# Optimization experiments

Measured on AMD Instinct MI355X. Metric: run time of the kernel, lower is better.

The kernel has to match this reference:

```python
import jax, jax.numpy as jnp
import numpy as np

N_NODES = 50000
N_EDGES = 800000
IN_DIM = 89
HID = 128


def gcn_conv(x, src, dst, deg_inv_sqrt, W, b):
    # PyG GCNConv: x' = D^{-1/2} (A + I) D^{-1/2} (x W) + b
    h = x @ W  # [N, F_out]
    norm = deg_inv_sqrt[src] * deg_inv_sqrt[dst]  # per-edge norm [E]
    msgs = h[src] * norm[:, None]  # gather + scale [E, F_out]
    agg = jax.ops.segment_sum(msgs, dst, num_segments=x.shape[0])
    # self-loop contribution: norm = deg_inv_sqrt[i]^2
    agg = agg + h * (deg_inv_sqrt * deg_inv_sqrt)[:, None]
    return agg + b


def setup_inputs() -> dict:
    key = jax.random.key(0)
    k1, k2, k3, k4, k5, k6 = jax.random.split(key, 6)
    x = jax.random.normal(k1, (N_NODES, IN_DIM), dtype=jnp.float32)
    edge_index = jax.random.randint(k2, (2, N_EDGES), 0, N_NODES, dtype=jnp.int64)
    # Glorot-style init for GCN weights
    W1 = jax.random.normal(k3, (IN_DIM, HID), dtype=jnp.float32) * (1.0 / np.sqrt(IN_DIM))
    b1 = jnp.zeros((HID,), dtype=jnp.float32)
    W2 = jax.random.normal(k4, (HID, HID), dtype=jnp.float32) * (1.0 / np.sqrt(HID))
    b2 = jnp.zeros((HID,), dtype=jnp.float32)
    return {"x": x, "edge_index": edge_index, "W1": W1, "b1": b1, "W2": W2, "b2": b2}


def reference(x, edge_index, W1, b1, W2, b2):
    src = edge_index[0]
    dst = edge_index[1]
    n = x.shape[0]
    # degree of A + I: 1 (self loop) + in-degree
    deg = 1.0 + jax.ops.segment_sum(jnp.ones((src.shape[0],), x.dtype), dst, num_segments=n)
    deg_inv_sqrt = jax.lax.rsqrt(deg)
    h = jax.nn.relu(gcn_conv(x, src, dst, deg_inv_sqrt, W1, b1))
    h = jax.nn.relu(gcn_conv(h, src, dst, deg_inv_sqrt, W2, b2))
    return (h, edge_index)
```

## Files before the change

### kernel.cpp

```cpp
#include <hip/hip_runtime.h>
#include <hip/hip_bf16.h>


#define HID 128
#define KIN 89
#define KP1 96
#define KP2 128
#define BSH 7
#define BNODES 128
#define MAXBUCK 512
#define NPB 128
#define P4CAP 3072

typedef __attribute__((ext_vector_type(8))) short bf16x8;
typedef __attribute__((ext_vector_type(4))) float f32x4;

static __device__ inline float2 unpack_bf16(unsigned v) {
    union { unsigned u; float f; } lo, hi;
    lo.u = v << 16;
    hi.u = v & 0xFFFF0000u;
    return make_float2(lo.f, hi.f);
}

static __device__ inline unsigned pack_bf16(float a, float b) {
    __hip_bfloat162 h = __float22bfloat162_rn(make_float2(a, b));
    return *reinterpret_cast<unsigned*>(&h);
}

static __device__ inline unsigned short f2bf(float v) {
    __hip_bfloat16 h = __float2bfloat16(v);
    return *reinterpret_cast<unsigned short*>(&h);
}

__global__ __launch_bounds__(256) void p1_kernel(
    const int* __restrict__ ei,
    int* __restrict__ histG,
    const float* __restrict__ W1, unsigned short* __restrict__ W1t,
    const float* __restrict__ W2, unsigned short* __restrict__ W2t,
    int E, int nbuck)
{
    __shared__ int h[MAXBUCK];
    const int tid = threadIdx.x, blk = blockIdx.x;
    const int* dst = ei + E;
    for (int b = tid; b < nbuck; b += 256) h[b] = 0;

    int tg = blk * 256 + tid;
    if (tg < HID * KP1) {
        int n = tg / KP1, k = tg % KP1;
        W1t[tg] = f2bf(k < KIN ? W1[(size_t)k * HID + n] : 0.0f);
    } else {
        int t2 = tg - HID * KP1;
        if (t2 < HID * HID) {
            int n = t2 / HID, k = t2 % HID;
            W2t[t2] = f2bf(W2[(size_t)k * HID + n]);
        }
    }
    __syncthreads();

    const int chunk = (E + NPB - 1) / NPB;
    const int beg = blk * chunk, end = min(beg + chunk, E);
    for (int i = beg + tid; i < end; i += 256)
        atomicAdd(&h[dst[i] >> BSH], 1);
    __syncthreads();
    for (int b = tid; b < nbuck; b += 256) histG[b * NPB + blk] = h[b];
}

__global__ __launch_bounds__(NPB) void p2a_kernel(
    int* __restrict__ histG, int* __restrict__ totals)
{
    __shared__ int wsum[NPB / 64];
    const int b = blockIdx.x, tid = threadIdx.x, lane = tid & 63, wid = tid >> 6;
    int c = histG[b * NPB + tid];
    int s = c;
#pragma unroll
    for (int off = 1; off < 64; off <<= 1) {
        int t = __shfl_up(s, off, 64);
        if (lane >= off) s += t;
    }
    if (lane == 63) wsum[wid] = s;
    __syncthreads();
    if (tid == 0) {
        int a = 0;
#pragma unroll
        for (int w = 0; w < NPB / 64; ++w) { int t = wsum[w]; wsum[w] = a; a += t; }
    }
    __syncthreads();
    int excl = wsum[wid] + s - c;
    histG[b * NPB + tid] = excl;
    if (tid == NPB - 1) totals[b] = excl + c;
}

static __device__ inline void scan_totals2(const int* __restrict__ totals,
                                           int* __restrict__ sexcl,
                                           int* __restrict__ wsum,
                                           int nbuck, int tid)
{
    const int lane = tid & 63, wid = tid >> 6;
    const int i0 = 2 * tid, i1 = 2 * tid + 1;
    int t0 = (i0 < nbuck) ? totals[i0] : 0;
    int t1 = (i1 < nbuck) ? totals[i1] : 0;
    int p = t0 + t1;
    int s = p;
#pragma unroll
    for (int off = 1; off < 64; off <<= 1) {
        int t = __shfl_up(s, off, 64);
        if (lane >= off) s += t;
    }
    if (lane == 63) wsum[wid] = s;
    __syncthreads();
    if (tid == 0) {
        int a = 0;
#pragma unroll
        for (int w = 0; w < 4; ++w) { int t = wsum[w]; wsum[w] = a; a += t; }
    }
    __syncthreads();
    int excl = wsum[wid] + s - p;
    sexcl[i0] = excl;
    sexcl[i1] = excl + t0;
}

__global__ __launch_bounds__(256) void p3_part_kernel(
    const int* __restrict__ ei, const int* __restrict__ histG,
    const int* __restrict__ totals, unsigned* __restrict__ ebuf,
    float* __restrict__ outE,
    int E, int nbuck)
{
    __shared__ int cur[MAXBUCK];
    __shared__ int wsum[4];
    const int tid = threadIdx.x, blk = blockIdx.x;
    const int* src = ei;
    const int* dst = ei + E;
    scan_totals2(totals, cur, wsum, nbuck, tid);
    __syncthreads();
    for (int b = tid; b < nbuck; b += 256) cur[b] += histG[b * NPB + blk];
    const int chunk = (E + NPB - 1) / NPB;
    const int beg = blk * chunk, end = min(beg + chunk, E);
    __syncthreads();
    for (int i = beg + tid; i < end; i += 256) {
        int sxi = src[i];
        int d = dst[i];
        int b = d >> BSH;
        int pos = atomicAdd(&cur[b], 1);
        ebuf[pos] = ((unsigned)(d & (BNODES - 1)) << 16) | (unsigned)sxi;
        outE[i] = (float)sxi;
        outE[E + i] = (float)d;
    }
}

__global__ __launch_bounds__(256) void p4_sort_kernel(
    const unsigned* __restrict__ ebuf, const int* __restrict__ totals,
    unsigned short* __restrict__ csr, int* __restrict__ rowptr,
    float* __restrict__ dis,
    const float* __restrict__ X, unsigned* __restrict__ Xhs,
    int N, int E, int nbuck)
{
    __shared__ int counts[BNODES];
    __shared__ int cursor[BNODES];
    __shared__ int sbase[MAXBUCK];
    __shared__ int wsum[4];
    __shared__ int w2[2];
    __shared__ unsigned short staging[P4CAP];
    const int b = blockIdx.x, tid = threadIdx.x, lane = tid & 63, wid = tid >> 6;

    scan_totals2(totals, sbase, wsum, nbuck, tid);
    __syncthreads();
    const int gbase = sbase[b];
    const int cnt = totals[b];

    if (tid < BNODES) counts[tid] = 0;
    __syncthreads();
    for (int i = tid; i < cnt; i += 256)
        atomicAdd(&counts[ebuf[gbase + i] >> 16], 1);
    __syncthreads();

    int c = 0, s = 0;
    if (tid < BNODES) {
        c = counts[tid];
        s = c;
#pragma unroll
        for (int off = 1; off < 64; off <<= 1) {
            int t = __shfl_up(s, off, 64);
            if (lane >= off) s += t;
        }
        if (lane == 63) w2[wid] = s;
    }
    __syncthreads();
    if (tid == 0) { int t = w2[0]; w2[0] = 0; w2[1] = t; }
    __syncthreads();
    if (tid < BNODES) {
        int excl = w2[wid] + s - c;
        cursor[tid] = excl;
        int node = b * BNODES + tid;
        if (node < N) {
            rowptr[node] = gbase + excl;
            dis[node] = rsqrtf(1.0f + (float)c);
        }
    }
    if (b == 0 && tid == 0) rowptr[N] = E;
    __syncthreads();

    if (cnt <= P4CAP) {
        for (int i = tid; i < cnt; i += 256) {
            unsigned v = ebuf[gbase + i];
            int pos = atomicAdd(&cursor[v >> 16], 1);
            staging[pos] = (unsigned short)(v & 0xFFFFu);
        }
        __syncthreads();
        for (int i = tid; i < cnt; i += 256)
            csr[gbase + i] = staging[i];
    } else {
        for (int i = tid; i < cnt; i += 256) {
            unsigned v = ebuf[gbase + i];
            int pos = atomicAdd(&cursor[v >> 16], 1);
            csr[gbase + pos] = (unsigned short)(v & 0xFFFFu);
        }
    }

    const int nloc = min(BNODES, N - b * BNODES);
    if (nloc > 0) {
        const int tot = nloc * (KP1 / 2);
        for (int i = tid; i < tot; i += 256) {
            int nl = i / (KP1 / 2), cc = i % (KP1 / 2);
            int node = b * BNODES + nl;
            float d = rsqrtf(1.0f + (float)counts[nl]);
            const float* xr = X + (size_t)node * KIN;
            float a = (2 * cc     < KIN) ? d * xr[2 * cc]     : 0.0f;
            float bb = (2 * cc + 1 < KIN) ? d * xr[2 * cc + 1] : 0.0f;
            Xhs[(size_t)node * (KP1 / 2) + cc] = pack_bf16(a, bb);
        }
    }
}

template<int KPA, bool LAYER1>
__global__ __launch_bounds__(256) void fused_kernel(
    const uint4* __restrict__ rows, const int* __restrict__ rowptr,
    const unsigned short* __restrict__ csr,
    const unsigned short* __restrict__ Wt, const float* __restrict__ bias,
    const float* __restrict__ dis, void* __restrict__ outp, int N)
{
    constexpr int ROWU4 = KPA / 8;
    constexpr int LDSP  = (KPA == 96) ? 104 : 136;
    __shared__ unsigned short lds_a[16][LDSP];
    const int tid  = threadIdx.x;
    const int wave = tid >> 6;
    const int lane = tid & 63;
    const int sub  = (lane >> 4) & 3;
    const int sl   = lane & 15;
    const int slc  = (ROWU4 == 16) ? sl : min(sl, ROWU4 - 1);
    const bool act = (ROWU4 == 16) || (sl < ROWU4);
    const int blk0 = blockIdx.x * 16;

    {
        const int lrow = wave * 4 + sub;
        const int node = blk0 + lrow;
        const bool valid = node < N;
        const int cn = valid ? node : N - 1;

        uint4 sv = rows[(size_t)cn * ROWU4 + slc];
        float a0, a1, a2, a3, a4, a5, a6, a7;
        {
            float2 q;
            q = unpack_bf16(sv.x); a0 = q.x; a1 = q.y;
            q = unpack_bf16(sv.y); a2 = q.x; a3 = q.y;
            q = unpack_bf16(sv.z); a4 = q.x; a5 = q.y;
            q = unpack_bf16(sv.w); a6 = q.x; a7 = q.y;
        }

        int beg = rowptr[cn];
        int end = valid ? rowptr[cn + 1] : beg;
        int j = beg;
        for (; j + 4 <= end; j += 4) {
            int r0 = csr[j], r1 = csr[j + 1], r2 = csr[j + 2], r3 = csr[j + 3];
            uint4 v0 = rows[(size_t)r0 * ROWU4 + slc];
            uint4 v1 = rows[(size_t)r1 * ROWU4 + slc];
            uint4 v2 = rows[(size_t)r2 * ROWU4 + slc];
            uint4 v3 = rows[(size_t)r3 * ROWU4 + slc];
            float2 q;
            q = unpack_bf16(v0.x); a0 += q.x; a1 += q.y;
            q = unpack_bf16(v0.y); a2 += q.x; a3 += q.y;
            q = unpack_bf16(v0.z); a4 += q.x; a5 += q.y;
            q = unpack_bf16(v0.w); a6 += q.x; a7 += q.y;
            q = unpack_bf16(v1.x); a0 += q.x; a1 += q.y;
            q = unpack_bf16(v1.y); a2 += q.x; a3 += q.y;
            q = unpack_bf16(v1.z); a4 += q.x; a5 += q.y;
            q = unpack_bf16(v1.w); a6 += q.x; a7 += q.y;
            q = unpack_bf16(v2.x); a0 += q.x; a1 += q.y;
            q = unpack_bf16(v2.y); a2 += q.x; a3 += q.y;
            q = unpack_bf16(v2.z); a4 += q.x; a5 += q.y;
            q = unpack_bf16(v2.w); a6 += q.x; a7 += q.y;
            q = unpack_bf16(v3.x); a0 += q.x; a1 += q.y;
            q = unpack_bf16(v3.y); a2 += q.x; a3 += q.y;
            q = unpack_bf16(v3.z); a4 += q.x; a5 += q.y;
            q = unpack_bf16(v3.w); a6 += q.x; a7 += q.y;
        }
        for (; j < end; ++j) {
            int r = csr[j];
            uint4 v = rows[(size_t)r * ROWU4 + slc];
            float2 q;
            q = unpack_bf16(v.x); a0 += q.x; a1 += q.y;
            q = unpack_bf16(v.y); a2 += q.x; a3 += q.y;
            q = unpack_bf16(v.z); a4 += q.x; a5 += q.y;
            q = unpack_bf16(v.w); a6 += q.x; a7 += q.y;
        }

        if (act) {
            uint4 pk = make_uint4(pack_bf16(a0, a1), pack_bf16(a2, a3),
                                  pack_bf16(a4, a5), pack_bf16(a6, a7));
            *(uint4*)&lds_a[lrow][sl * 8] = pk;
        }
    }
    __syncthreads();

    const int m    = lane & 15;
    const int quad = lane >> 4;
    const int node = blk0 + m;

    f32x4 acc[2];
    acc[0] = (f32x4){0.0f, 0.0f, 0.0f, 0.0f};
    acc[1] = (f32x4){0.0f, 0.0f, 0.0f, 0.0f};

    const unsigned short* arp = &lds_a[m][0];

#pragma unroll
    for (int c = 0; c < KPA / 32; ++c) {
        const int k0 = c * 32 + quad * 8;
        bf16x8 nv = *(const bf16x8*)(arp + k0);
#pragma unroll
        for (int t2 = 0; t2 < 2; ++t2) {
            const int t = wave * 2 + t2;
            bf16x8 wv = *(const bf16x8*)(Wt + (size_t)(t * 16 + m) * KPA + k0);
            acc[t2] = __builtin_amdgcn_mfma_f32_16x16x32_bf16(wv, nv, acc[t2], 0, 0, 0);
        }
    }

    if (node < N) {
        const float dv = dis[node];
#pragma unroll
        for (int t2 = 0; t2 < 2; ++t2) {
            const int col0 = (wave * 2 + t2) * 16 + quad * 4;
            float4 bb = *(const float4*)&bias[col0];
            float r0 = fmaxf(fmaf(dv, acc[t2][0], bb.x), 0.0f);
            float r1 = fmaxf(fmaf(dv, acc[t2][1], bb.y), 0.0f);
            float r2 = fmaxf(fmaf(dv, acc[t2][2], bb.z), 0.0f);
            float r3 = fmaxf(fmaf(dv, acc[t2][3], bb.w), 0.0f);
            if (LAYER1) {
                uint2 u;
                u.x = pack_bf16(r0 * dv, r1 * dv);
                u.y = pack_bf16(r2 * dv, r3 * dv);
                *(uint2*)((unsigned short*)outp + (size_t)node * HID + col0) = u;
            } else {
                float4 r = make_float4(r0, r1, r2, r3);
                *(float4*)((float*)outp + (size_t)node * HID + col0) = r;
            }
        }
    }
}


static inline char* wsal(char*& p, size_t n) {
    uintptr_t q = ((uintptr_t)p + 255) & ~(uintptr_t)255;
    char* r = (char*)q;
    p = r + n;
    return r;
}

extern "C" void kernel_launch(void* const* d_in, const int* in_sizes, int n_in,
                              void* d_out, int out_size, void* d_ws, size_t ws_size,
                              hipStream_t stream) {
    const float* x  = (const float*)d_in[0];
    const int*   ei = (const int*)d_in[1];
    const float* W1 = (const float*)d_in[2];
    const float* b1 = (const float*)d_in[3];
    const float* W2 = (const float*)d_in[4];
    const float* b2 = (const float*)d_in[5];

    const int N = in_sizes[0] / KIN;
    const int E = in_sizes[1] / 2;
    const int nbuck = (N + BNODES - 1) >> BSH;

    float* out  = (float*)d_out;
    float* outH = out;
    float* outE = out + (size_t)N * HID;

    char* ws = (char*)d_ws;
    int*            histG  = (int*)wsal(ws, (size_t)MAXBUCK * NPB * 4);
    int*            totals = (int*)wsal(ws, MAXBUCK * 4);
    int*            rowptr = (int*)wsal(ws, (size_t)(N + 1) * 4);
    float*          dis    = (float*)wsal(ws, (size_t)N * 4);
    unsigned*       ebuf   = (unsigned*)wsal(ws, (size_t)E * 4);
    unsigned short* csr    = (unsigned short*)wsal(ws, (size_t)E * 2);
    unsigned*       Xhs    = (unsigned*)wsal(ws, (size_t)N * (KP1 / 2) * 4);
    unsigned short* g2h    = (unsigned short*)wsal(ws, (size_t)N * HID * 2);
    unsigned short* W1t    = (unsigned short*)wsal(ws, (size_t)HID * KP1 * 2);
    unsigned short* W2t    = (unsigned short*)wsal(ws, (size_t)HID * HID * 2);

    p1_kernel<<<NPB, 256, 0, stream>>>(ei, histG, W1, W1t, W2, W2t, E, nbuck);
    p2a_kernel<<<nbuck, NPB, 0, stream>>>(histG, totals);
    p3_part_kernel<<<NPB, 256, 0, stream>>>(ei, histG, totals, ebuf, outE,
                                            E, nbuck);
    p4_sort_kernel<<<nbuck, 256, 0, stream>>>(ebuf, totals, csr, rowptr, dis,
                                              x, Xhs, N, E, nbuck);

    const int ngf = (N + 15) / 16;

    fused_kernel<KP1, true><<<ngf, 256, 0, stream>>>(
        (const uint4*)Xhs, rowptr, csr, W1t, b1, dis, g2h, N);

    fused_kernel<KP2, false><<<ngf, 256, 0, stream>>>(
        (const uint4*)g2h, rowptr, csr, W2t, b2, dis, outH, N);
}
```

Before: 197.2 us.

## Sort nodes by in-degree so fused aggregation blocks get balanced work

Builds a degree histogram in the sort kernel, scans it, and scatters node ids into a degree-ordered permutation. The fused aggregation+GEMM kernels then process nodes through this permutation, so each 16-node block and each wave handles nodes of similar degree and less time is lost to divergence from uneven edge counts. This adds two small kernels, extra atomics, and an indirection. It also scatters row reads and output writes, which loses locality between neighbouring nodes.

```diff
diff --git a/kernel.cpp b/kernel.cpp
--- a/kernel.cpp
+++ b/kernel.cpp
@@ -11,6 +11,7 @@
 #define MAXBUCK 512
 #define NPB 128
 #define P4CAP 3072
+#define DMAX 64
 
 typedef __attribute__((ext_vector_type(8))) short bf16x8;
 typedef __attribute__((ext_vector_type(4))) float f32x4;
@@ -34,7 +35,7 @@
 
 __global__ __launch_bounds__(256) void p1_kernel(
     const int* __restrict__ ei,
-    int* __restrict__ histG,
+    int* __restrict__ histG, int* __restrict__ dhist,
     const float* __restrict__ W1, unsigned short* __restrict__ W1t,
     const float* __restrict__ W2, unsigned short* __restrict__ W2t,
     int E, int nbuck)
@@ -43,6 +44,7 @@
     const int tid = threadIdx.x, blk = blockIdx.x;
     const int* dst = ei + E;
     for (int b = tid; b < nbuck; b += 256) h[b] = 0;
+    if (blk == 0 && tid < DMAX) dhist[tid] = 0;
 
     int tg = blk * 256 + tid;
     if (tg < HID * KP1) {
@@ -152,6 +154,7 @@
     unsigned short* __restrict__ csr, int* __restrict__ rowptr,
     float* __restrict__ dis,
     const float* __restrict__ X, unsigned* __restrict__ Xhs,
+    int* __restrict__ dhist,
     int N, int E, int nbuck)
 {
     __shared__ int counts[BNODES];
@@ -194,6 +197,7 @@
         if (node < N) {
             rowptr[node] = gbase + excl;
             dis[node] = rsqrtf(1.0f + (float)c);
+            atomicAdd(&dhist[min(c, DMAX - 1)], 1);
         }
     }
     if (b == 0 && tid == 0) rowptr[N] = E;
@@ -231,10 +235,29 @@
     }
 }
 
+__global__ __launch_bounds__(64) void p5_scan_kernel(int* __restrict__ dhist)
+{
+    if (threadIdx.x == 0) {
+        int a = 0;
+        for (int i = 0; i < DMAX; ++i) { int t = dhist[i]; dhist[i] = a; a += t; }
+    }
+}
+
+__global__ __launch_bounds__(256) void p6_perm_kernel(
+    const int* __restrict__ rowptr, int* __restrict__ dhist,
+    int* __restrict__ perm, int N)
+{
+    int n = blockIdx.x * 256 + threadIdx.x;
+    if (n >= N) return;
+    int deg = rowptr[n + 1] - rowptr[n];
+    int pos = atomicAdd(&dhist[min(deg, DMAX - 1)], 1);
+    perm[pos] = n;
+}
+
 template<int KPA, bool LAYER1>
 __global__ __launch_bounds__(256) void fused_kernel(
     const uint4* __restrict__ rows, const int* __restrict__ rowptr,
-    const unsigned short* __restrict__ csr,
+    const unsigned short* __restrict__ csr, const int* __restrict__ perm,
     const unsigned short* __restrict__ Wt, const float* __restrict__ bias,
     const float* __restrict__ dis, void* __restrict__ outp, int N)
 {
@@ -252,9 +275,9 @@
 
     {
         const int lrow = wave * 4 + sub;
-        const int node = blk0 + lrow;
-        const bool valid = node < N;
-        const int cn = valid ? node : N - 1;
+        const int gidx = blk0 + lrow;
+        const bool valid = gidx < N;
+        const int cn = perm[valid ? gidx : N - 1];
 
         uint4 sv = rows[(size_t)cn * ROWU4 + slc];
         float a0, a1, a2, a3, a4, a5, a6, a7;
@@ -313,7 +336,8 @@
 
     const int m    = lane & 15;
     const int quad = lane >> 4;
-    const int node = blk0 + m;
+    const int gidx2 = blk0 + m;
+    const int node = perm[min(gidx2, N - 1)];
 
     f32x4 acc[2];
     acc[0] = (f32x4){0.0f, 0.0f, 0.0f, 0.0f};
@@ -333,7 +357,7 @@
         }
     }
 
-    if (node < N) {
+    if (gidx2 < N) {
         const float dv = dis[node];
 #pragma unroll
         for (int t2 = 0; t2 < 2; ++t2) {
@@ -393,19 +417,24 @@
     unsigned short* g2h    = (unsigned short*)wsal(ws, (size_t)N * HID * 2);
     unsigned short* W1t    = (unsigned short*)wsal(ws, (size_t)HID * KP1 * 2);
     unsigned short* W2t    = (unsigned short*)wsal(ws, (size_t)HID * HID * 2);
-
-    p1_kernel<<<NPB, 256, 0, stream>>>(ei, histG, W1, W1t, W2, W2t, E, nbuck);
+    int*            dhist  = (int*)wsal(ws, DMAX * 4);
+    int*            perm   = (int*)wsal(ws, (size_t)N * 4);
+
+    p1_kernel<<<NPB, 256, 0, stream>>>(ei, histG, dhist, W1, W1t, W2, W2t,
+                                       E, nbuck);
     p2a_kernel<<<nbuck, NPB, 0, stream>>>(histG, totals);
     p3_part_kernel<<<NPB, 256, 0, stream>>>(ei, histG, totals, ebuf, outE,
                                             E, nbuck);
     p4_sort_kernel<<<nbuck, 256, 0, stream>>>(ebuf, totals, csr, rowptr, dis,
-                                              x, Xhs, N, E, nbuck);
+                                              x, Xhs, dhist, N, E, nbuck);
+    p5_scan_kernel<<<1, 64, 0, stream>>>(dhist);
+    p6_perm_kernel<<<(N + 255) / 256, 256, 0, stream>>>(rowptr, dhist, perm, N);
 
     const int ngf = (N + 15) / 16;
 
     fused_kernel<KP1, true><<<ngf, 256, 0, stream>>>(
-        (const uint4*)Xhs, rowptr, csr, W1t, b1, dis, g2h, N);
+        (const uint4*)Xhs, rowptr, csr, perm, W1t, b1, dis, g2h, N);
 
     fused_kernel<KP2, false><<<ngf, 256, 0, stream>>>(
-        (const uint4*)g2h, rowptr, csr, W2t, b2, dis, outH, N);
-}
+        (const uint4*)g2h, rowptr, csr, perm, W2t, b2, dis, outH, N);
+}
```

Result: slower. 459.5 us (+133.1%).
